# Optimization experiments

Measured on AMD Instinct MI355X. Metric: run time of the kernel, lower is better.

Reference implementation:

```python
import jax, jax.numpy as jnp
import numpy as np

ACTION_WEIGHT = 10.0
ACTION_DIM = 4
OBS_DIM = 128


def setup_inputs() -> dict:
    key = jax.random.key(0)
    k1, k2 = jax.random.split(key)
    B, H, T = 64, 32, ACTION_DIM + 256 * OBS_DIM  # 32772
    preds = jax.random.normal(k1, (B, H, T), dtype=jnp.float32)
    targ = jax.random.normal(k2, (B, H, T), dtype=jnp.float32)
    return {"preds": preds, "targ": targ}


def _chamfer(x, y):
    # x: [G, Nx, D] (gts), y: [G, Ny, D] (preds)
    # P[g, i, j] = ||x_i||^2 + ||y_j||^2 - 2 x_i . y_j
    x2 = jnp.sum(x * x, axis=-1)          # [G, Nx]
    y2 = jnp.sum(y * y, axis=-1)          # [G, Ny]
    zz = jnp.einsum('gnd,gmd->gnm', x, y)  # [G, Nx, Ny]
    P = x2[:, :, None] + y2[:, None, :] - 2.0 * zz
    loss_1 = jnp.sum(jnp.min(P, axis=1), axis=1)  # min over x points, sum over y points
    loss_2 = jnp.sum(jnp.min(P, axis=2), axis=1)  # min over y points, sum over x points
    return loss_1 + loss_2  # [G]


def reference(preds, targ):
    B, H, T = preds.shape
    actions = preds[:, :, :ACTION_DIM]
    action_targs = targ[:, :, :ACTION_DIM]
    action_loss = jnp.mean((actions - action_targs) ** 2, axis=-1)  # [B, H]
    a0_loss = jnp.mean(action_loss[:, 0])
    action_loss = action_loss.at[:, 0].multiply(ACTION_WEIGHT)
    action_loss = jnp.mean(action_loss)

    obs = preds[:, :, ACTION_DIM:].reshape(B, H, -1, OBS_DIM)
    obs_targ = targ[:, :, ACTION_DIM:].reshape(B, H, -1, OBS_DIM)
    N = obs.shape[2]
    # Vectorize the per-horizon loop: fold (B, H) into one batched dim.
    x = obs_targ.reshape(B * H, N, OBS_DIM)
    y = obs.reshape(B * H, N, OBS_DIM)
    ch = _chamfer(x, y)  # [B*H]
    # sum_h mean_b(ch[:, h]) / H == mean over (B*H)
    chamfer_loss = jnp.mean(ch)

    return (action_loss + chamfer_loss, a0_loss)
```

## Files before the change

### kernel.cpp

```cpp
#include <hip/hip_runtime.h>
#include <hip/hip_bf16.h>

#define T_DIM 32772
#define NGROUP 2048

typedef short short8v __attribute__((ext_vector_type(8)));
typedef float float4v __attribute__((ext_vector_type(4)));
typedef unsigned int uint4v __attribute__((ext_vector_type(4)));

__device__ __forceinline__ unsigned int f2bf2(float a, float b) {
    __hip_bfloat162 h = __float22bfloat162_rn(make_float2(a, b));
    union { __hip_bfloat162 h; unsigned int u; } c; c.h = h;
    return c.u;
}

__device__ __forceinline__ short8v pack8(const float4v u0, const float4v u1) {
    uint4v p;
    p[0] = f2bf2(u0[0], u0[1]);
    p[1] = f2bf2(u0[2], u0[3]);
    p[2] = f2bf2(u1[0], u1[1]);
    p[3] = f2bf2(u1[2], u1[3]);
    return __builtin_bit_cast(short8v, p);
}

__global__ __launch_bounds__(512) void chamfer_kernel(
    const float* __restrict__ preds, const float* __restrict__ targ,
    float* __restrict__ ch_out)
{
    __shared__ __align__(16) unsigned short Ys[2][64 * 128];
    __shared__ float y2s[256];
    __shared__ float colmin_w[8][256];
    __shared__ float redA[8];
    __shared__ float redB[4];

    const int g = blockIdx.x;
    const float* gx = targ  + (size_t)g * T_DIM + 4;
    const float* gy = preds + (size_t)g * T_DIM + 4;

    const int tid  = threadIdx.x;
    const int lane = tid & 63;
    const int w    = tid >> 6;
    const int lg   = lane >> 4;
    const int lc   = lane & 15;

    const int prow = tid >> 3;
    const int pcb  = tid & 7;
    char* Ysb = (char*)Ys;
    const int wslot = ((pcb + prow) & 7) << 4;
    const int woffA = prow * 256 + wslot;
    const int woffB = prow * 256 + 128 + wslot;

    float4v pf0, pf1, pf2, pf3;
    {
        const float* src = gy + (size_t)prow * 128 + pcb * 8;
        pf0 = *reinterpret_cast<const float4v*>(src);
        pf1 = *reinterpret_cast<const float4v*>(src + 4);
        pf2 = *reinterpret_cast<const float4v*>(src + 64);
        pf3 = *reinterpret_cast<const float4v*>(src + 68);
    }

    short8v a_frag[2][4];
    float x2r[2][4];
    #pragma unroll
    for (int ti = 0; ti < 2; ++ti) {
        const float* xr = gx + (size_t)(w * 32 + ti * 16 + lc) * 128;
        float ss = 0.f;
        #pragma unroll
        for (int kk = 0; kk < 4; ++kk) {
            const float4v u0 = *reinterpret_cast<const float4v*>(xr + kk * 32 + lg * 8);
            const float4v u1 = *reinterpret_cast<const float4v*>(xr + kk * 32 + lg * 8 + 4);
            ss += u0[0]*u0[0] + u0[1]*u0[1] + u0[2]*u0[2] + u0[3]*u0[3];
            ss += u1[0]*u1[0] + u1[1]*u1[1] + u1[2]*u1[2] + u1[3]*u1[3];
            a_frag[ti][kk] = pack8(u0, u1);
        }
        ss += __shfl_xor(ss, 16);
        ss += __shfl_xor(ss, 32);
        #pragma unroll
        for (int r = 0; r < 4; ++r)
            x2r[ti][r] = __shfl(ss, lg * 4 + r);
    }

    {
        float ss = pf0[0]*pf0[0]+pf0[1]*pf0[1]+pf0[2]*pf0[2]+pf0[3]*pf0[3]
                 + pf1[0]*pf1[0]+pf1[1]*pf1[1]+pf1[2]*pf1[2]+pf1[3]*pf1[3]
                 + pf2[0]*pf2[0]+pf2[1]*pf2[1]+pf2[2]*pf2[2]+pf2[3]*pf2[3]
                 + pf3[0]*pf3[0]+pf3[1]*pf3[1]+pf3[2]*pf3[2]+pf3[3]*pf3[3];
        ss += __shfl_xor(ss, 1);
        ss += __shfl_xor(ss, 2);
        ss += __shfl_xor(ss, 4);
        if (pcb == 0) y2s[prow] = ss;
        *reinterpret_cast<short8v*>(Ysb + woffA) = pack8(pf0, pf1);
        *reinterpret_cast<short8v*>(Ysb + woffB) = pack8(pf2, pf3);
    }
    __syncthreads();

    float rowmin[2][4];
    #pragma unroll
    for (int ti = 0; ti < 2; ++ti)
        #pragma unroll
        for (int r = 0; r < 4; ++r) rowmin[ti][r] = 1e30f;
    float cmin[4];

    const int rs0 = ((lg + lc) & 7) << 4;
    const int rs1 = ((lg + lc + 4) & 7) << 4;

    #pragma unroll
    for (int c = 0; c < 4; ++c) {
        if (c < 3) {
            const float* src = gy + (size_t)((c + 1) * 64 + prow) * 128 + pcb * 8;
            pf0 = *reinterpret_cast<const float4v*>(src);
            pf1 = *reinterpret_cast<const float4v*>(src + 4);
            pf2 = *reinterpret_cast<const float4v*>(src + 64);
            pf3 = *reinterpret_cast<const float4v*>(src + 68);
        }

        char* buf = Ysb + (c & 1) * 16384;
        #pragma unroll
        for (int tjl = 0; tjl < 4; ++tjl) {
            const int tj = c * 4 + tjl;
            const int rbyte = (tjl * 16 + lc) * 256;
            short8v b_frag[4];
            b_frag[0] = *reinterpret_cast<const short8v*>(buf + rbyte + rs0);
            b_frag[1] = *reinterpret_cast<const short8v*>(buf + rbyte + rs1);
            b_frag[2] = *reinterpret_cast<const short8v*>(buf + rbyte + 128 + rs0);
            b_frag[3] = *reinterpret_cast<const short8v*>(buf + rbyte + 128 + rs1);

            const float y2c = y2s[tj * 16 + lc];
            float cminv = 1e30f;
            #pragma unroll
            for (int ti = 0; ti < 2; ++ti) {
                float4v acc = {0.f, 0.f, 0.f, 0.f};
                #pragma unroll
                for (int kk = 0; kk < 4; ++kk)
                    acc = __builtin_amdgcn_mfma_f32_16x16x32_bf16(
                        a_frag[ti][kk], b_frag[kk], acc, 0, 0, 0);
                #pragma unroll
                for (int r = 0; r < 4; ++r) {
                    const float P = (x2r[ti][r] + y2c) - 2.0f * acc[r];
                    rowmin[ti][r] = fminf(rowmin[ti][r], P);
                    cminv = fminf(cminv, P);
                }
            }
            cminv = fminf(cminv, __shfl_xor(cminv, 16));
            cminv = fminf(cminv, __shfl_xor(cminv, 32));
            if (lg == tjl) cmin[c] = cminv;
        }

        if (c < 3) {
            float ss = pf0[0]*pf0[0]+pf0[1]*pf0[1]+pf0[2]*pf0[2]+pf0[3]*pf0[3]
                     + pf1[0]*pf1[0]+pf1[1]*pf1[1]+pf1[2]*pf1[2]+pf1[3]*pf1[3]
                     + pf2[0]*pf2[0]+pf2[1]*pf2[1]+pf2[2]*pf2[2]+pf2[3]*pf2[3]
                     + pf3[0]*pf3[0]+pf3[1]*pf3[1]+pf3[2]*pf3[2]+pf3[3]*pf3[3];
            ss += __shfl_xor(ss, 1);
            ss += __shfl_xor(ss, 2);
            ss += __shfl_xor(ss, 4);
            if (pcb == 0) y2s[(c + 1) * 64 + prow] = ss;
            char* wbuf = Ysb + ((c + 1) & 1) * 16384;
            *reinterpret_cast<short8v*>(wbuf + woffA) = pack8(pf0, pf1);
            *reinterpret_cast<short8v*>(wbuf + woffB) = pack8(pf2, pf3);
            __syncthreads();
        }
    }

    #pragma unroll
    for (int s = 0; s < 4; ++s)
        colmin_w[w][s * 64 + lane] = cmin[s];

    float s2 = 0.f;
    #pragma unroll
    for (int ti = 0; ti < 2; ++ti)
        #pragma unroll
        for (int r = 0; r < 4; ++r) {
            float v = rowmin[ti][r];
            v = fminf(v, __shfl_xor(v, 1));
            v = fminf(v, __shfl_xor(v, 2));
            v = fminf(v, __shfl_xor(v, 4));
            v = fminf(v, __shfl_xor(v, 8));
            s2 += v;
        }
    s2 += __shfl_xor(s2, 16);
    s2 += __shfl_xor(s2, 32);
    if (lane == 0) redA[w] = s2;
    __syncthreads();

    if (tid < 256) {
        float m = colmin_w[0][tid];
        #pragma unroll
        for (int ww = 1; ww < 8; ++ww) m = fminf(m, colmin_w[ww][tid]);
        #pragma unroll
        for (int s = 1; s < 64; s <<= 1) m += __shfl_xor(m, s);
        if (lane == 0) redB[w] = m;
    }
    __syncthreads();
    if (tid == 0) {
        const float l1 = redB[0] + redB[1] + redB[2] + redB[3];
        float l2 = 0.f;
        #pragma unroll
        for (int ww = 0; ww < 8; ++ww) l2 += redA[ww];
        ch_out[g] = l1 + l2;
    }
}

__global__ __launch_bounds__(256) void final_kernel(
    const float* __restrict__ preds, const float* __restrict__ targ,
    const float* __restrict__ ch, float* __restrict__ out)
{
    __shared__ float rsw[4], rsa[4], rsc[4];
    const int tid = threadIdx.x;
    const int lane = tid & 63, w = tid >> 6;
    float sw = 0.f, sa0 = 0.f, sc = 0.f;
    for (int p = tid; p < NGROUP; p += 256) {
        const float* pp = preds + (size_t)p * T_DIM;
        const float* tt = targ  + (size_t)p * T_DIM;
        float al = 0.f;
        #pragma unroll
        for (int d = 0; d < 4; ++d) { const float df = pp[d] - tt[d]; al += df * df; }
        al *= 0.25f;
        if ((p & 31) == 0) { sw += 10.f * al; sa0 += al; }
        else               { sw += al; }
        sc += ch[p];
    }
    #pragma unroll
    for (int s = 1; s < 64; s <<= 1) {
        sw  += __shfl_xor(sw, s);
        sa0 += __shfl_xor(sa0, s);
        sc  += __shfl_xor(sc, s);
    }
    if (lane == 0) { rsw[w] = sw; rsa[w] = sa0; rsc[w] = sc; }
    __syncthreads();
    if (tid == 0) {
        float tsw = 0.f, tsa = 0.f, tsc = 0.f;
        #pragma unroll
        for (int i = 0; i < 4; ++i) { tsw += rsw[i]; tsa += rsa[i]; tsc += rsc[i]; }
        out[0] = tsw / 2048.f + tsc / 2048.f;
        out[1] = tsa / 64.f;
    }
}

extern "C" void kernel_launch(void* const* d_in, const int* in_sizes, int n_in,
                              void* d_out, int out_size, void* d_ws, size_t ws_size,
                              hipStream_t stream) {
    const float* preds = (const float*)d_in[0];
    const float* targ  = (const float*)d_in[1];
    float* out = (float*)d_out;
    float* ch  = (float*)d_ws;
    chamfer_kernel<<<NGROUP, 512, 0, stream>>>(preds, targ, ch);
    final_kernel<<<1, 256, 0, stream>>>(preds, targ, ch, out);
}
```

Baseline: 128.3 us.

## Cut registers and LDS in chamfer kernel to raise occupancy, hoist norm terms

Drops the register-held next-chunk prefetch in favour of a load-then-sync per chunk, and moves x-norms from per-lane registers into shared memory. It aliases the column-min scratch onto the Y staging buffer to shrink LDS, and adds a higher minimum-occupancy launch bound. The per-element work is also cut: the x2 and y2 terms are pulled out of the min operations and added once after the reductions. MFMA calls are interleaved across two accumulators. The aim is more resident blocks to hide memory latency, at the cost of losing explicit global-load/compute overlap within a block.

```diff
diff --git a/kernel.cpp b/kernel.cpp
--- a/kernel.cpp
+++ b/kernel.cpp
@@ -23,15 +23,16 @@
     return __builtin_bit_cast(short8v, p);
 }
 
-__global__ __launch_bounds__(512) void chamfer_kernel(
+__global__ __launch_bounds__(512, 8) void chamfer_kernel(
     const float* __restrict__ preds, const float* __restrict__ targ,
     float* __restrict__ ch_out)
 {
     __shared__ __align__(16) unsigned short Ys[2][64 * 128];
     __shared__ float y2s[256];
-    __shared__ float colmin_w[8][256];
+    __shared__ float x2s[256];
     __shared__ float redA[8];
     __shared__ float redB[4];
+    float* colmin_alias = reinterpret_cast<float*>(&Ys[0][0]);
 
     const int g = blockIdx.x;
     const float* gx = targ  + (size_t)g * T_DIM + 4;
@@ -50,17 +51,7 @@
     const int woffA = prow * 256 + wslot;
     const int woffB = prow * 256 + 128 + wslot;
 
-    float4v pf0, pf1, pf2, pf3;
-    {
-        const float* src = gy + (size_t)prow * 128 + pcb * 8;
-        pf0 = *reinterpret_cast<const float4v*>(src);
-        pf1 = *reinterpret_cast<const float4v*>(src + 4);
-        pf2 = *reinterpret_cast<const float4v*>(src + 64);
-        pf3 = *reinterpret_cast<const float4v*>(src + 68);
-    }
-
     short8v a_frag[2][4];
-    float x2r[2][4];
     #pragma unroll
     for (int ti = 0; ti < 2; ++ti) {
         const float* xr = gx + (size_t)(w * 32 + ti * 16 + lc) * 128;
@@ -75,24 +66,8 @@
         }
         ss += __shfl_xor(ss, 16);
         ss += __shfl_xor(ss, 32);
-        #pragma unroll
-        for (int r = 0; r < 4; ++r)
-            x2r[ti][r] = __shfl(ss, lg * 4 + r);
-    }
-
-    {
-        float ss = pf0[0]*pf0[0]+pf0[1]*pf0[1]+pf0[2]*pf0[2]+pf0[3]*pf0[3]
-                 + pf1[0]*pf1[0]+pf1[1]*pf1[1]+pf1[2]*pf1[2]+pf1[3]*pf1[3]
-                 + pf2[0]*pf2[0]+pf2[1]*pf2[1]+pf2[2]*pf2[2]+pf2[3]*pf2[3]
-                 + pf3[0]*pf3[0]+pf3[1]*pf3[1]+pf3[2]*pf3[2]+pf3[3]*pf3[3];
-        ss += __shfl_xor(ss, 1);
-        ss += __shfl_xor(ss, 2);
-        ss += __shfl_xor(ss, 4);
-        if (pcb == 0) y2s[prow] = ss;
-        *reinterpret_cast<short8v*>(Ysb + woffA) = pack8(pf0, pf1);
-        *reinterpret_cast<short8v*>(Ysb + woffB) = pack8(pf2, pf3);
-    }
-    __syncthreads();
+        if (lg == 0) x2s[w * 32 + ti * 16 + lc] = ss;
+    }
 
     float rowmin[2][4];
     #pragma unroll
@@ -103,50 +78,16 @@
 
     const int rs0 = ((lg + lc) & 7) << 4;
     const int rs1 = ((lg + lc + 4) & 7) << 4;
+    const int x2byte = (w * 32 + lg * 4) * 4;
 
     #pragma unroll
     for (int c = 0; c < 4; ++c) {
-        if (c < 3) {
-            const float* src = gy + (size_t)((c + 1) * 64 + prow) * 128 + pcb * 8;
-            pf0 = *reinterpret_cast<const float4v*>(src);
-            pf1 = *reinterpret_cast<const float4v*>(src + 4);
-            pf2 = *reinterpret_cast<const float4v*>(src + 64);
-            pf3 = *reinterpret_cast<const float4v*>(src + 68);
-        }
-
-        char* buf = Ysb + (c & 1) * 16384;
-        #pragma unroll
-        for (int tjl = 0; tjl < 4; ++tjl) {
-            const int tj = c * 4 + tjl;
-            const int rbyte = (tjl * 16 + lc) * 256;
-            short8v b_frag[4];
-            b_frag[0] = *reinterpret_cast<const short8v*>(buf + rbyte + rs0);
-            b_frag[1] = *reinterpret_cast<const short8v*>(buf + rbyte + rs1);
-            b_frag[2] = *reinterpret_cast<const short8v*>(buf + rbyte + 128 + rs0);
-            b_frag[3] = *reinterpret_cast<const short8v*>(buf + rbyte + 128 + rs1);
-
-            const float y2c = y2s[tj * 16 + lc];
-            float cminv = 1e30f;
-            #pragma unroll
-            for (int ti = 0; ti < 2; ++ti) {
-                float4v acc = {0.f, 0.f, 0.f, 0.f};
-                #pragma unroll
-                for (int kk = 0; kk < 4; ++kk)
-                    acc = __builtin_amdgcn_mfma_f32_16x16x32_bf16(
-                        a_frag[ti][kk], b_frag[kk], acc, 0, 0, 0);
-                #pragma unroll
-                for (int r = 0; r < 4; ++r) {
-                    const float P = (x2r[ti][r] + y2c) - 2.0f * acc[r];
-                    rowmin[ti][r] = fminf(rowmin[ti][r], P);
-                    cminv = fminf(cminv, P);
-                }
-            }
-            cminv = fminf(cminv, __shfl_xor(cminv, 16));
-            cminv = fminf(cminv, __shfl_xor(cminv, 32));
-            if (lg == tjl) cmin[c] = cminv;
-        }
-
-        if (c < 3) {
+        {
+            const float* src = gy + (size_t)(c * 64 + prow) * 128 + pcb * 8;
+            const float4v pf0 = *reinterpret_cast<const float4v*>(src);
+            const float4v pf1 = *reinterpret_cast<const float4v*>(src + 4);
+            const float4v pf2 = *reinterpret_cast<const float4v*>(src + 64);
+            const float4v pf3 = *reinterpret_cast<const float4v*>(src + 68);
             float ss = pf0[0]*pf0[0]+pf0[1]*pf0[1]+pf0[2]*pf0[2]+pf0[3]*pf0[3]
                      + pf1[0]*pf1[0]+pf1[1]*pf1[1]+pf1[2]*pf1[2]+pf1[3]*pf1[3]
                      + pf2[0]*pf2[0]+pf2[1]*pf2[1]+pf2[2]*pf2[2]+pf2[3]*pf2[3]
@@ -154,21 +95,70 @@
             ss += __shfl_xor(ss, 1);
             ss += __shfl_xor(ss, 2);
             ss += __shfl_xor(ss, 4);
-            if (pcb == 0) y2s[(c + 1) * 64 + prow] = ss;
-            char* wbuf = Ysb + ((c + 1) & 1) * 16384;
+            if (pcb == 0) y2s[c * 64 + prow] = ss;
+            char* wbuf = Ysb + (c & 1) * 16384;
             *reinterpret_cast<short8v*>(wbuf + woffA) = pack8(pf0, pf1);
             *reinterpret_cast<short8v*>(wbuf + woffB) = pack8(pf2, pf3);
-            __syncthreads();
+        }
+        __syncthreads();
+
+        char* buf = Ysb + (c & 1) * 16384;
+        #pragma unroll
+        for (int tjl = 0; tjl < 4; ++tjl) {
+            const int tj = c * 4 + tjl;
+            const int rbyte = (tjl * 16 + lc) * 256;
+            const float y2c = y2s[tj * 16 + lc];
+
+            float4v acc0 = {0.f, 0.f, 0.f, 0.f};
+            float4v acc1 = {0.f, 0.f, 0.f, 0.f};
+            {
+                short8v b0 = *reinterpret_cast<const short8v*>(buf + rbyte + rs0);
+                short8v b1 = *reinterpret_cast<const short8v*>(buf + rbyte + rs1);
+                acc0 = __builtin_amdgcn_mfma_f32_16x16x32_bf16(a_frag[0][0], b0, acc0, 0, 0, 0);
+                acc1 = __builtin_amdgcn_mfma_f32_16x16x32_bf16(a_frag[1][0], b0, acc1, 0, 0, 0);
+                acc0 = __builtin_amdgcn_mfma_f32_16x16x32_bf16(a_frag[0][1], b1, acc0, 0, 0, 0);
+                acc1 = __builtin_amdgcn_mfma_f32_16x16x32_bf16(a_frag[1][1], b1, acc1, 0, 0, 0);
+                b0 = *reinterpret_cast<const short8v*>(buf + rbyte + 128 + rs0);
+                b1 = *reinterpret_cast<const short8v*>(buf + rbyte + 128 + rs1);
+                acc0 = __builtin_amdgcn_mfma_f32_16x16x32_bf16(a_frag[0][2], b0, acc0, 0, 0, 0);
+                acc1 = __builtin_amdgcn_mfma_f32_16x16x32_bf16(a_frag[1][2], b0, acc1, 0, 0, 0);
+                acc0 = __builtin_amdgcn_mfma_f32_16x16x32_bf16(a_frag[0][3], b1, acc0, 0, 0, 0);
+                acc1 = __builtin_amdgcn_mfma_f32_16x16x32_bf16(a_frag[1][3], b1, acc1, 0, 0, 0);
+            }
+
+            float cminv = 1e30f;
+            {
+                const float4v x2v = *reinterpret_cast<const float4v*>((char*)x2s + x2byte);
+                #pragma unroll
+                for (int r = 0; r < 4; ++r) {
+                    const float t = -2.0f * acc0[r];
+                    rowmin[0][r] = fminf(rowmin[0][r], y2c + t);
+                    cminv = fminf(cminv, x2v[r] + t);
+                }
+            }
+            {
+                const float4v x2v = *reinterpret_cast<const float4v*>((char*)x2s + x2byte + 64);
+                #pragma unroll
+                for (int r = 0; r < 4; ++r) {
+                    const float t = -2.0f * acc1[r];
+                    rowmin[1][r] = fminf(rowmin[1][r], y2c + t);
+                    cminv = fminf(cminv, x2v[r] + t);
+                }
+            }
+            cminv = fminf(cminv, __shfl_xor(cminv, 16));
+            cminv = fminf(cminv, __shfl_xor(cminv, 32));
+            if (lg == tjl) cmin[c] = cminv;
         }
     }
 
     #pragma unroll
     for (int s = 0; s < 4; ++s)
-        colmin_w[w][s * 64 + lane] = cmin[s];
+        colmin_alias[w * 256 + s * 64 + lane] = cmin[s];
 
     float s2 = 0.f;
     #pragma unroll
-    for (int ti = 0; ti < 2; ++ti)
+    for (int ti = 0; ti < 2; ++ti) {
+        const float4v x2v = *reinterpret_cast<const float4v*>((char*)x2s + x2byte + ti * 64);
         #pragma unroll
         for (int r = 0; r < 4; ++r) {
             float v = rowmin[ti][r];
@@ -176,17 +166,19 @@
             v = fminf(v, __shfl_xor(v, 2));
             v = fminf(v, __shfl_xor(v, 4));
             v = fminf(v, __shfl_xor(v, 8));
-            s2 += v;
-        }
+            s2 += x2v[r] + v;
+        }
+    }
     s2 += __shfl_xor(s2, 16);
     s2 += __shfl_xor(s2, 32);
     if (lane == 0) redA[w] = s2;
     __syncthreads();
 
     if (tid < 256) {
-        float m = colmin_w[0][tid];
-        #pragma unroll
-        for (int ww = 1; ww < 8; ++ww) m = fminf(m, colmin_w[ww][tid]);
+        float m = colmin_alias[tid];
+        #pragma unroll
+        for (int ww = 1; ww < 8; ++ww) m = fminf(m, colmin_alias[ww * 256 + tid]);
+        m += y2s[tid];
         #pragma unroll
         for (int s = 1; s < 64; s <<= 1) m += __shfl_xor(m, s);
         if (lane == 0) redB[w] = m;
```

New measurement: 484.0 us. 277% more time.
